# Optimization experiments

Hardware: AMD Instinct MI355X
Metric: run time of the kernel (lower is better)

The kernel has to match this reference:

```python
import jax, jax.numpy as jnp
import numpy as np

N = 100000
E = 3200000
F_IN = 256
HID = 128


def _dconv_k1(x_cat, w, b):
    # torch_geometric_temporal DConv with K=1:
    # H = X @ W[0,0] + X @ W[1,0] + b   (no graph propagation for K=1)
    return x_cat @ (w[0, 0] + w[1, 0]) + b


def _dcrnn_cell(x, h, wz, bz, wr, br, wh, bh):
    xh = jnp.concatenate([x, h], axis=1)
    z = jax.nn.sigmoid(_dconv_k1(xh, wz, bz))
    r = jax.nn.sigmoid(_dconv_k1(xh, wr, br))
    xrh = jnp.concatenate([x, r * h], axis=1)
    h_tilde = jnp.tanh(_dconv_k1(xrh, wh, bh))
    return z * h + (1.0 - z) * h_tilde


def setup_inputs() -> dict:
    key = jax.random.key(0)
    ks = jax.random.split(key, 16)

    def gw(k, shape):
        fan_in = shape[-2]
        return jax.random.normal(k, shape, dtype=jnp.float32) / np.sqrt(fan_in)

    inp = {
        "x": jax.random.normal(ks[0], (N, F_IN), dtype=jnp.float32),
        "edge_index": jax.random.randint(ks[1], (2, E), 0, N, dtype=jnp.int64 if jax.config.jax_enable_x64 else jnp.int32),
        "edge_weight": jax.random.uniform(ks[2], (E,), dtype=jnp.float32),
        "w_z1": gw(ks[3], (2, 1, F_IN + HID, HID)), "b_z1": jnp.zeros((HID,), jnp.float32),
        "w_r1": gw(ks[4], (2, 1, F_IN + HID, HID)), "b_r1": jnp.zeros((HID,), jnp.float32),
        "w_h1": gw(ks[5], (2, 1, F_IN + HID, HID)), "b_h1": jnp.zeros((HID,), jnp.float32),
        "w_z2": gw(ks[6], (2, 1, HID + HID // 2, HID // 2)), "b_z2": jnp.zeros((HID // 2,), jnp.float32),
        "w_r2": gw(ks[7], (2, 1, HID + HID // 2, HID // 2)), "b_r2": jnp.zeros((HID // 2,), jnp.float32),
        "w_h2": gw(ks[8], (2, 1, HID + HID // 2, HID // 2)), "b_h2": jnp.zeros((HID // 2,), jnp.float32),
        "w_lin1": gw(ks[9], (HID // 2, 16)), "b_lin1": jnp.zeros((16,), jnp.float32),
        "w_lin2": gw(ks[10], (16, 1)), "b_lin2": jnp.zeros((1,), jnp.float32),
    }
    return inp


def reference(x, edge_index, edge_weight,
              w_z1, b_z1, w_r1, b_r1, w_h1, b_h1,
              w_z2, b_z2, w_r2, b_r2, w_h2, b_h2,
              w_lin1, b_lin1, w_lin2, b_lin2):
    # edge_index / edge_weight are unused in the K=1 DConv math (faithful to tgt source).
    h0 = jnp.zeros((x.shape[0], w_z1.shape[-1]), x.dtype)
    h = _dcrnn_cell(x, h0, w_z1, b_z1, w_r1, b_r1, w_h1, b_h1)
    h = jax.nn.relu(h)
    h0b = jnp.zeros((x.shape[0], w_z2.shape[-1]), x.dtype)
    h = _dcrnn_cell(h, h0b, w_z2, b_z2, w_r2, b_r2, w_h2, b_h2)
    h = jax.nn.relu(h)
    # Dropout(0.2) is identity at inference
    h = jax.nn.relu(h @ w_lin1 + b_lin1)
    return h @ w_lin2 + b_lin2
```

## Files before the change

kernel.cpp:

```cpp
#include <hip/hip_runtime.h>

typedef _Float16 f16;
typedef _Float16 f16x4 __attribute__((ext_vector_type(4)));
typedef _Float16 f16x8 __attribute__((ext_vector_type(8)));
typedef float    f32x4 __attribute__((ext_vector_type(4)));

#define N_ROWS 100000
#define RT 1563
#define LSX 40
#define LSH1 136
#define LSH2 72

#define W1T_OFF 0
#define W1T_BYTES (256 * 256 * 2)
#define W2T_OFF W1T_BYTES

#define XS0 0
#define XS1 5120
#define ARENA 26624
#define H1S 0
#define H2S 17408

__global__ void prep_w(const float* __restrict__ wz1, const float* __restrict__ wh1,
                       const float* __restrict__ wz2, const float* __restrict__ wh2,
                       f16* __restrict__ W1T, f16* __restrict__ W2T) {
    const int b = blockIdx.x;
    if (b < 256) {
        int idx = b * 256 + threadIdx.x;
        int k = idx >> 8, c = idx & 255;
        const float* w = (c < 128) ? wz1 : wh1;
        int cc = c & 127;
        W1T[c * 256 + k] = (f16)(w[k * 128 + cc] + w[384 * 128 + k * 128 + cc]);
    } else {
        int idx = (b - 256) * 256 + threadIdx.x;
        int k = idx >> 7, c = idx & 127;
        const float* w = (c < 64) ? wz2 : wh2;
        int cc = c & 63;
        W2T[c * 128 + k] = (f16)(w[k * 64 + cc] + w[192 * 64 + k * 64 + cc]);
    }
}

__global__ __launch_bounds__(256, 3) void fused(
    const float* __restrict__ x,
    const f16* __restrict__ W1T, const f16* __restrict__ W2T,
    const float* __restrict__ bz1, const float* __restrict__ bh1,
    const float* __restrict__ bz2, const float* __restrict__ bh2,
    const float* __restrict__ wl1, const float* __restrict__ bl1,
    const float* __restrict__ wl2, const float* __restrict__ bl2,
    float* __restrict__ out)
{
    __shared__ __align__(16) char arena[ARENA];
    const int tid = threadIdx.x, lane = tid & 63, wave = tid >> 6;
    const int ln = lane & 15, quad = lane >> 4;
    const int r0 = blockIdx.x * 64;

    const int xr = tid >> 2, xcg = tid & 3;
    int gxr = r0 + xr; if (gxr >= N_ROWS) gxr = N_ROWS - 1;
    const float* xp = x + (size_t)gxr * 256 + (xcg << 3);

    const int Mz = 2 * wave;

    const f16* wb[4];
#pragma unroll
    for (int mi = 0; mi < 4; ++mi) {
        const int M = (mi < 2) ? (Mz + mi) : (8 + Mz + mi - 2);
        wb[mi] = W1T + (size_t)(M * 16 + ln) * 256 + quad * 8;
    }

    f32x4 acc[4][4];
#pragma unroll
    for (int a = 0; a < 4; ++a)
#pragma unroll
        for (int b = 0; b < 4; ++b) acc[a][b] = (f32x4){0.f, 0.f, 0.f, 0.f};

    float4 pxa0, pxb0, pxa1, pxb1;
    f16x8 afp[4], afn[4];

    pxa0 = *(const float4*)(xp + 0);  pxb0 = *(const float4*)(xp + 4);
    pxa1 = *(const float4*)(xp + 32); pxb1 = *(const float4*)(xp + 36);
#pragma unroll
    for (int mi = 0; mi < 4; ++mi) afp[mi] = *(const f16x8*)(wb[mi]);

#pragma unroll
    for (int it = 0; it < 8; ++it) {
        f16* XsB = (f16*)(arena + ((it & 1) ? XS1 : XS0));
        const float4 ca = (it & 1) ? pxa1 : pxa0;
        const float4 cb = (it & 1) ? pxb1 : pxb0;
        *(f16x8*)&XsB[xr * LSX + (xcg << 3)] =
            (f16x8){(f16)ca.x,(f16)ca.y,(f16)ca.z,(f16)ca.w,
                    (f16)cb.x,(f16)cb.y,(f16)cb.z,(f16)cb.w};
        __syncthreads();
        if (it < 6) {
            if (it & 1) { pxa1 = *(const float4*)(xp + (it + 2) * 32);
                          pxb1 = *(const float4*)(xp + (it + 2) * 32 + 4); }
            else        { pxa0 = *(const float4*)(xp + (it + 2) * 32);
                          pxb0 = *(const float4*)(xp + (it + 2) * 32 + 4); }
        }
        if (it < 7) {
#pragma unroll
            for (int mi = 0; mi < 4; ++mi)
                afn[mi] = *(const f16x8*)(wb[mi] + (it + 1) * 32);
        }
        __builtin_amdgcn_sched_barrier(0);

        f16x8 bf[4];
#pragma unroll
        for (int nt = 0; nt < 4; ++nt)
            bf[nt] = *(const f16x8*)&XsB[(16 * nt + ln) * LSX + quad * 8];
#pragma unroll
        for (int mi = 0; mi < 4; ++mi)
#pragma unroll
            for (int nt = 0; nt < 4; ++nt)
                acc[mi][nt] = __builtin_amdgcn_mfma_f32_16x16x32_f16(afp[mi], bf[nt], acc[mi][nt], 0, 0, 0);
#pragma unroll
        for (int mi = 0; mi < 4; ++mi) afp[mi] = afn[mi];
    }
    __syncthreads();

    f16x8 w2f[2][4];
#pragma unroll
    for (int kc = 0; kc < 4; ++kc) {
        w2f[0][kc] = *(const f16x8*)(W2T + (size_t)(16 * wave + ln) * 128 + kc * 32 + quad * 8);
        w2f[1][kc] = *(const f16x8*)(W2T + (size_t)(64 + 16 * wave + ln) * 128 + kc * 32 + quad * 8);
    }

    f16* h1s = (f16*)(arena + H1S);
#pragma unroll
    for (int mi = 0; mi < 2; ++mi) {
        const int jg0 = 32 * wave + 16 * mi + (quad << 2);
        const float4 zb = *(const float4*)(bz1 + jg0);
        const float4 hb = *(const float4*)(bh1 + jg0);
#pragma unroll
        for (int nt = 0; nt < 4; ++nt) {
            const int row = 16 * nt + ln;
            f16x4 pk;
#pragma unroll
            for (int i = 0; i < 4; ++i) {
                float zp = acc[mi][nt][i]     + (&zb.x)[i];
                float hp = acc[mi + 2][nt][i] + (&hb.x)[i];
                float ex = __expf(2.0f * hp);
                float th = 1.0f - 2.0f / (ex + 1.0f);
                float sg = 1.0f / (1.0f + __expf(zp));
                pk[i] = (f16)fmaxf(th * sg, 0.0f);
            }
            *(f16x4*)&h1s[row * LSH1 + jg0] = pk;
        }
    }
    __syncthreads();

    f32x4 acc2[2][4];
#pragma unroll
    for (int a = 0; a < 2; ++a)
#pragma unroll
        for (int b = 0; b < 4; ++b) acc2[a][b] = (f32x4){0.f, 0.f, 0.f, 0.f};
#pragma unroll
    for (int kc = 0; kc < 4; ++kc) {
        f16x8 bf[4];
#pragma unroll
        for (int nt = 0; nt < 4; ++nt)
            bf[nt] = *(const f16x8*)&h1s[(16 * nt + ln) * LSH1 + kc * 32 + quad * 8];
#pragma unroll
        for (int m = 0; m < 2; ++m)
#pragma unroll
            for (int nt = 0; nt < 4; ++nt)
                acc2[m][nt] = __builtin_amdgcn_mfma_f32_16x16x32_f16(w2f[m][kc], bf[nt], acc2[m][nt], 0, 0, 0);
    }
    __syncthreads();

    f16* h2s = (f16*)(arena + H2S);
    {
        const int jg0 = 16 * wave + (quad << 2);
        const float4 zb = *(const float4*)(bz2 + jg0);
        const float4 hb = *(const float4*)(bh2 + jg0);
#pragma unroll
        for (int nt = 0; nt < 4; ++nt) {
            const int row = 16 * nt + ln;
            f16x4 pk;
#pragma unroll
            for (int i = 0; i < 4; ++i) {
                float zp = acc2[0][nt][i] + (&zb.x)[i];
                float hp = acc2[1][nt][i] + (&hb.x)[i];
                float ex = __expf(2.0f * hp);
                float th = 1.0f - 2.0f / (ex + 1.0f);
                float sg = 1.0f / (1.0f + __expf(zp));
                pk[i] = (f16)fmaxf(th * sg, 0.0f);
            }
            *(f16x4*)&h2s[row * LSH2 + jg0] = pk;
        }
    }
    __syncthreads();

    const float blv = bl1[ln], wlv = wl2[ln], bl2v = bl2[0];
    f16x8 bfr[2];
#pragma unroll
    for (int kc = 0; kc < 2; ++kc)
#pragma unroll
        for (int j = 0; j < 8; ++j)
            bfr[kc][j] = (f16)wl1[(32 * kc + 8 * quad + j) * 16 + ln];

    f32x4 acc3 = (f32x4){0.f, 0.f, 0.f, 0.f};
#pragma unroll
    for (int kc = 0; kc < 2; ++kc) {
        f16x8 af = *(const f16x8*)&h2s[(16 * wave + ln) * LSH2 + kc * 32 + quad * 8];
        acc3 = __builtin_amdgcn_mfma_f32_16x16x32_f16(af, bfr[kc], acc3, 0, 0, 0);
    }
#pragma unroll
    for (int i = 0; i < 4; ++i) {
        float v = fmaxf(acc3[i] + blv, 0.0f) * wlv;
        v += __shfl_xor(v, 1);
        v += __shfl_xor(v, 2);
        v += __shfl_xor(v, 4);
        v += __shfl_xor(v, 8);
        if (ln == 0) {
            const int row = r0 + 16 * wave + (quad << 2) + i;
            if (row < N_ROWS) out[row] = v + bl2v;
        }
    }
}

extern "C" void kernel_launch(void* const* d_in, const int* in_sizes, int n_in,
                              void* d_out, int out_size, void* d_ws, size_t ws_size,
                              hipStream_t stream) {
    const float* x   = (const float*)d_in[0];
    const float* wz1 = (const float*)d_in[3];
    const float* bz1 = (const float*)d_in[4];
    const float* wh1 = (const float*)d_in[7];
    const float* bh1 = (const float*)d_in[8];
    const float* wz2 = (const float*)d_in[9];
    const float* bz2 = (const float*)d_in[10];
    const float* wh2 = (const float*)d_in[13];
    const float* bh2 = (const float*)d_in[14];
    const float* wl1 = (const float*)d_in[15];
    const float* bl1 = (const float*)d_in[16];
    const float* wl2 = (const float*)d_in[17];
    const float* bl2 = (const float*)d_in[18];

    char* ws = (char*)d_ws;
    f16* W1T = (f16*)(ws + W1T_OFF);
    f16* W2T = (f16*)(ws + W2T_OFF);
    float* out = (float*)d_out;

    prep_w<<<320, 256, 0, stream>>>(wz1, wh1, wz2, wh2, W1T, W2T);
    fused<<<RT, 256, 0, stream>>>(x, W1T, W2T, bz1, bh1, bz2, bh2,
                                  wl1, bl1, wl2, bl2, out);
}
```

Measured before the change: 228.4 us.

## Stage full X tile in LDS upfront, merge gate divisions, raise occupancy

The kernel now loads the whole 64x256 fp32 X tile into registers at once, converts it to fp16 and writes it to a single LDS buffer. This replaces the per-chunk double-buffered staging and the __syncthreads it needed on every K step. The gate math is fused so two divisions become one hardware reciprocal, with a clamp on the tanh input to avoid overflow. The launch-bounds occupancy target goes from 3 to 4 blocks per CU, and one barrier between layer-2 MMA and the h2 store is dropped because the two regions don't overlap. The prep kernel's index mapping is swapped so W1T/W2T writes are coalesced. Risks: more register pressure from the upfront X loads, and weight loads are no longer prefetched ahead of the MFMAs.

Result: slower. 236.3 us (+3.4%).

```diff
diff --git a/kernel.cpp b/kernel.cpp
--- a/kernel.cpp
+++ b/kernel.cpp
@@ -7,7 +7,7 @@
 
 #define N_ROWS 100000
 #define RT 1563
-#define LSX 40
+#define LSX 264
 #define LSH1 136
 #define LSH2 72
 
@@ -15,9 +15,7 @@
 #define W1T_BYTES (256 * 256 * 2)
 #define W2T_OFF W1T_BYTES
 
-#define XS0 0
-#define XS1 5120
-#define ARENA 26624
+#define ARENA 33792
 #define H1S 0
 #define H2S 17408
 
@@ -27,20 +25,27 @@
     const int b = blockIdx.x;
     if (b < 256) {
         int idx = b * 256 + threadIdx.x;
-        int k = idx >> 8, c = idx & 255;
+        int c = idx >> 8, k = idx & 255;
         const float* w = (c < 128) ? wz1 : wh1;
         int cc = c & 127;
         W1T[c * 256 + k] = (f16)(w[k * 128 + cc] + w[384 * 128 + k * 128 + cc]);
     } else {
         int idx = (b - 256) * 256 + threadIdx.x;
-        int k = idx >> 7, c = idx & 127;
+        int c = idx >> 7, k = idx & 127;
         const float* w = (c < 64) ? wz2 : wh2;
         int cc = c & 63;
         W2T[c * 128 + k] = (f16)(w[k * 64 + cc] + w[192 * 64 + k * 64 + cc]);
     }
 }
 
-__global__ __launch_bounds__(256, 3) void fused(
+__device__ __forceinline__ float gate(float zp, float hp) {
+    float e2h = __expf(2.0f * fminf(hp, 15.0f));
+    float ez  = __expf(zp);
+    float r   = __builtin_amdgcn_rcpf((e2h + 1.0f) * (1.0f + ez));
+    return fmaxf((e2h - 1.0f) * r, 0.0f);
+}
+
+__global__ __launch_bounds__(256, 4) void fused(
     const float* __restrict__ x,
     const f16* __restrict__ W1T, const f16* __restrict__ W2T,
     const float* __restrict__ bz1, const float* __restrict__ bh1,
@@ -58,8 +63,24 @@
     int gxr = r0 + xr; if (gxr >= N_ROWS) gxr = N_ROWS - 1;
     const float* xp = x + (size_t)gxr * 256 + (xcg << 3);
 
+    f16* Xs = (f16*)arena;
+
+    {
+        float4 xa[8], xb[8];
+#pragma unroll
+        for (int kc = 0; kc < 8; ++kc) {
+            xa[kc] = *(const float4*)(xp + kc * 32);
+            xb[kc] = *(const float4*)(xp + kc * 32 + 4);
+        }
+#pragma unroll
+        for (int kc = 0; kc < 8; ++kc) {
+            *(f16x8*)&Xs[xr * LSX + kc * 32 + (xcg << 3)] =
+                (f16x8){(f16)xa[kc].x,(f16)xa[kc].y,(f16)xa[kc].z,(f16)xa[kc].w,
+                        (f16)xb[kc].x,(f16)xb[kc].y,(f16)xb[kc].z,(f16)xb[kc].w};
+        }
+    }
+
     const int Mz = 2 * wave;
-
     const f16* wb[4];
 #pragma unroll
     for (int mi = 0; mi < 4; ++mi) {
@@ -67,53 +88,28 @@
         wb[mi] = W1T + (size_t)(M * 16 + ln) * 256 + quad * 8;
     }
 
+    __syncthreads();
+
     f32x4 acc[4][4];
 #pragma unroll
     for (int a = 0; a < 4; ++a)
 #pragma unroll
         for (int b = 0; b < 4; ++b) acc[a][b] = (f32x4){0.f, 0.f, 0.f, 0.f};
 
-    float4 pxa0, pxb0, pxa1, pxb1;
-    f16x8 afp[4], afn[4];
-
-    pxa0 = *(const float4*)(xp + 0);  pxb0 = *(const float4*)(xp + 4);
-    pxa1 = *(const float4*)(xp + 32); pxb1 = *(const float4*)(xp + 36);
-#pragma unroll
-    for (int mi = 0; mi < 4; ++mi) afp[mi] = *(const f16x8*)(wb[mi]);
-
 #pragma unroll
     for (int it = 0; it < 8; ++it) {
-        f16* XsB = (f16*)(arena + ((it & 1) ? XS1 : XS0));
-        const float4 ca = (it & 1) ? pxa1 : pxa0;
-        const float4 cb = (it & 1) ? pxb1 : pxb0;
-        *(f16x8*)&XsB[xr * LSX + (xcg << 3)] =
-            (f16x8){(f16)ca.x,(f16)ca.y,(f16)ca.z,(f16)ca.w,
-                    (f16)cb.x,(f16)cb.y,(f16)cb.z,(f16)cb.w};
-        __syncthreads();
-        if (it < 6) {
-            if (it & 1) { pxa1 = *(const float4*)(xp + (it + 2) * 32);
-                          pxb1 = *(const float4*)(xp + (it + 2) * 32 + 4); }
-            else        { pxa0 = *(const float4*)(xp + (it + 2) * 32);
-                          pxb0 = *(const float4*)(xp + (it + 2) * 32 + 4); }
-        }
-        if (it < 7) {
-#pragma unroll
-            for (int mi = 0; mi < 4; ++mi)
-                afn[mi] = *(const f16x8*)(wb[mi] + (it + 1) * 32);
-        }
-        __builtin_amdgcn_sched_barrier(0);
-
-        f16x8 bf[4];
+        f16x8 af[4], bf[4];
+#pragma unroll
+        for (int mi = 0; mi < 4; ++mi)
+            af[mi] = *(const f16x8*)(wb[mi] + it * 32);
 #pragma unroll
         for (int nt = 0; nt < 4; ++nt)
-            bf[nt] = *(const f16x8*)&XsB[(16 * nt + ln) * LSX + quad * 8];
+            bf[nt] = *(const f16x8*)&Xs[(16 * nt + ln) * LSX + it * 32 + quad * 8];
 #pragma unroll
         for (int mi = 0; mi < 4; ++mi)
 #pragma unroll
             for (int nt = 0; nt < 4; ++nt)
-                acc[mi][nt] = __builtin_amdgcn_mfma_f32_16x16x32_f16(afp[mi], bf[nt], acc[mi][nt], 0, 0, 0);
-#pragma unroll
-        for (int mi = 0; mi < 4; ++mi) afp[mi] = afn[mi];
+                acc[mi][nt] = __builtin_amdgcn_mfma_f32_16x16x32_f16(af[mi], bf[nt], acc[mi][nt], 0, 0, 0);
     }
     __syncthreads();
 
@@ -135,14 +131,9 @@
             const int row = 16 * nt + ln;
             f16x4 pk;
 #pragma unroll
-            for (int i = 0; i < 4; ++i) {
-                float zp = acc[mi][nt][i]     + (&zb.x)[i];
-                float hp = acc[mi + 2][nt][i] + (&hb.x)[i];
-                float ex = __expf(2.0f * hp);
-                float th = 1.0f - 2.0f / (ex + 1.0f);
-                float sg = 1.0f / (1.0f + __expf(zp));
-                pk[i] = (f16)fmaxf(th * sg, 0.0f);
-            }
+            for (int i = 0; i < 4; ++i)
+                pk[i] = (f16)gate(acc[mi][nt][i] + (&zb.x)[i],
+                                  acc[mi + 2][nt][i] + (&hb.x)[i]);
             *(f16x4*)&h1s[row * LSH1 + jg0] = pk;
         }
     }
@@ -165,7 +156,6 @@
             for (int nt = 0; nt < 4; ++nt)
                 acc2[m][nt] = __builtin_amdgcn_mfma_f32_16x16x32_f16(w2f[m][kc], bf[nt], acc2[m][nt], 0, 0, 0);
     }
-    __syncthreads();
 
     f16* h2s = (f16*)(arena + H2S);
     {
@@ -177,14 +167,9 @@
             const int row = 16 * nt + ln;
             f16x4 pk;
 #pragma unroll
-            for (int i = 0; i < 4; ++i) {
-                float zp = acc2[0][nt][i] + (&zb.x)[i];
-                float hp = acc2[1][nt][i] + (&hb.x)[i];
-                float ex = __expf(2.0f * hp);
-                float th = 1.0f - 2.0f / (ex + 1.0f);
-                float sg = 1.0f / (1.0f + __expf(zp));
-                pk[i] = (f16)fmaxf(th * sg, 0.0f);
-            }
+            for (int i = 0; i < 4; ++i)
+                pk[i] = (f16)gate(acc2[0][nt][i] + (&zb.x)[i],
+                                  acc2[1][nt][i] + (&hb.x)[i]);
             *(f16x4*)&h2s[row * LSH2 + jg0] = pk;
         }
     }
```
